# Optimization experiments

Measured on AMD Instinct MI355X. Metric: run time of the kernel, lower is better.

## Reference

```python
import jax, jax.numpy as jnp
import numpy as np

LN_EPS = 1e-3  # keras LayerNormalization default


def setup_inputs() -> dict:
    key = jax.random.key(0)
    k1, k2, k3 = jax.random.split(key, 3)
    B, T, D, H = 64, 512, 256, 512
    inputs = jax.random.normal(k1, (B, T, D), dtype=jnp.float32)
    h0 = jnp.zeros((B, H), dtype=jnp.float32)
    Wx = jax.random.normal(k2, (D, H), dtype=jnp.float32) / np.sqrt(D)
    Wh = jax.random.normal(k3, (H, H), dtype=jnp.float32) / np.sqrt(H)
    b = jnp.zeros((H,), dtype=jnp.float32)
    gamma = jnp.ones((H,), dtype=jnp.float32)
    beta = jnp.zeros((H,), dtype=jnp.float32)
    return {"inputs": inputs, "h0": h0, "Wx": Wx, "Wh": Wh, "b": b,
            "gamma": gamma, "beta": beta}


def _layer_norm(x, gamma, beta):
    mu = jnp.mean(x, axis=-1, keepdims=True)
    var = jnp.mean(jnp.square(x - mu), axis=-1, keepdims=True)
    return (x - mu) * jax.lax.rsqrt(var + LN_EPS) * gamma + beta


def reference(inputs, h0, Wx, Wh, b, gamma, beta):
    # Precompute input projection for all timesteps: [B, T, H]
    xproj = jnp.einsum('btd,dh->bth', inputs, Wx) + b

    def step(h, xp_t):
        z = xp_t + h @ Wh                      # SimpleRNNCell, activation=None
        h_new = jnp.tanh(_layer_norm(z, gamma, beta))
        return h_new, h_new

    _, outs = jax.lax.scan(step, h0, jnp.swapaxes(xproj, 0, 1))
    return jnp.swapaxes(outs, 0, 1)            # [B, T, H]
```

## Files before the change

### kernel.cpp

```cpp
#include <hip/hip_runtime.h>
#include <cstdint>
#include <cstddef>

#define T_STEPS 512
#define D_DIM 256
#define H_DIM 512
#define B_SZ 64

#define NCG 4
#define CGW (H_DIM / NCG)
#define NTH 512


#define BM 64
#define BN 128
#define BK 32

__global__ __launch_bounds__(256)
void xproj_gemm(const float* __restrict__ A, const float* __restrict__ Bm,
                const float* __restrict__ bias, float* __restrict__ C,
                int M, int N, int K) {
    __shared__ float As[BK][BM];
    __shared__ float Bs[BK][BN];

    const int tid = threadIdx.x;
    const int tx = tid & 15;
    const int ty = tid >> 4;
    const int row0 = blockIdx.y * BM;
    const int col0 = blockIdx.x * BN;

    float acc[4][8];
    #pragma unroll
    for (int i = 0; i < 4; ++i)
        #pragma unroll
        for (int j = 0; j < 8; ++j) acc[i][j] = 0.0f;

    for (int kt = 0; kt < K; kt += BK) {
        #pragma unroll
        for (int i = 0; i < 2; ++i) {
            int q  = tid + i * 256;
            int m  = q >> 3;
            int k4 = (q & 7) << 2;
            float4 v = *(const float4*)&A[(size_t)(row0 + m) * K + kt + k4];
            As[k4 + 0][m] = v.x; As[k4 + 1][m] = v.y;
            As[k4 + 2][m] = v.z; As[k4 + 3][m] = v.w;
        }
        #pragma unroll
        for (int i = 0; i < 4; ++i) {
            int q  = tid + i * 256;
            int kk = q >> 5;
            int n4 = (q & 31) << 2;
            *(float4*)&Bs[kk][n4] = *(const float4*)&Bm[(size_t)(kt + kk) * N + col0 + n4];
        }
        __syncthreads();
        #pragma unroll
        for (int k = 0; k < BK; ++k) {
            float4 a  = *(const float4*)&As[k][ty << 2];
            float4 b0 = *(const float4*)&Bs[k][tx << 2];
            float4 b1 = *(const float4*)&Bs[k][(tx << 2) + 64];
            float av[4] = {a.x, a.y, a.z, a.w};
            float bv[8] = {b0.x, b0.y, b0.z, b0.w, b1.x, b1.y, b1.z, b1.w};
            #pragma unroll
            for (int i = 0; i < 4; ++i)
                #pragma unroll
                for (int j = 0; j < 8; ++j)
                    acc[i][j] = fmaf(av[i], bv[j], acc[i][j]);
        }
        __syncthreads();
    }

    float bv0[4], bv1[4];
    #pragma unroll
    for (int j = 0; j < 4; ++j) {
        bv0[j] = bias[col0 + (tx << 2) + j];
        bv1[j] = bias[col0 + (tx << 2) + 64 + j];
    }
    #pragma unroll
    for (int i = 0; i < 4; ++i) {
        int r = row0 + (ty << 2) + i;
        float4 o0 = make_float4(acc[i][0] + bv0[0], acc[i][1] + bv0[1],
                                acc[i][2] + bv0[2], acc[i][3] + bv0[3]);
        float4 o1 = make_float4(acc[i][4] + bv1[0], acc[i][5] + bv1[1],
                                acc[i][6] + bv1[2], acc[i][7] + bv1[3]);
        *(float4*)&C[(size_t)r * N + col0 + (tx << 2)]      = o0;
        *(float4*)&C[(size_t)r * N + col0 + (tx << 2) + 64] = o1;
    }
}

__device__ __forceinline__ float tanh_fast(float x) {
    float ax = fabsf(x);
    float e  = __expf(2.0f * ax);
    float t  = 1.0f - 2.0f / (e + 1.0f);
    return copysignf(t, x);
}

__global__ __launch_bounds__(NTH)
void rnn_scan3(const float* __restrict__ Wh, const float* __restrict__ h0,
               const float* __restrict__ gamma, const float* __restrict__ beta,
               float* __restrict__ out,
               unsigned long long* __restrict__ zbuf) {
    const int r   = blockIdx.x & (B_SZ - 1);
    const int cg  = blockIdx.x >> 6;
    const int tid = threadIdx.x;
    const int c   = tid & (CGW - 1);
    const int kc  = tid >> 7;

    __shared__ float h_s[H_DIM];
    __shared__ float part_s[NCG][CGW];
    __shared__ float wred_s[16];

    float w[128];
    #pragma unroll
    for (int j = 0; j < 128; ++j)
        w[j] = Wh[(size_t)(kc * 128 + j) * H_DIM + cg * CGW + c];

    h_s[tid] = h0[r * H_DIM + tid];
    const float g_own = gamma[tid];
    const float b_own = beta[tid];
    float* outrow = out + (size_t)r * T_STEPS * H_DIM;
    unsigned long long* zrow0 = zbuf + (size_t)(r * 2) * H_DIM;
    __syncthreads();

    for (int t = 0; t < T_STEPS; ++t) {
        unsigned long long* zrow = zrow0 + (size_t)(t & 1) * H_DIM;
        const unsigned int tag = (unsigned int)(t + 1);

        float xp = 0.0f;
        if (tid < CGW) xp = outrow[t * H_DIM + cg * CGW + tid];

        float acc = 0.0f;
        const float4* h4 = (const float4*)&h_s[kc * 128];
        #pragma unroll
        for (int j4 = 0; j4 < 32; ++j4) {
            float4 hv = h4[j4];
            acc = fmaf(w[4 * j4 + 0], hv.x, acc);
            acc = fmaf(w[4 * j4 + 1], hv.y, acc);
            acc = fmaf(w[4 * j4 + 2], hv.z, acc);
            acc = fmaf(w[4 * j4 + 3], hv.w, acc);
        }
        part_s[kc][c] = acc;
        __syncthreads();

        if (tid < CGW) {
            float z = xp + part_s[0][tid] + part_s[1][tid]
                         + part_s[2][tid] + part_s[3][tid];
            unsigned long long pkt =
                ((unsigned long long)tag << 32) | (unsigned long long)__float_as_uint(z);
            __hip_atomic_store(&zrow[cg * CGW + tid], pkt,
                               __ATOMIC_RELAXED, __HIP_MEMORY_SCOPE_AGENT);
        }

        unsigned long long pkt;
        do {
            pkt = __hip_atomic_load(&zrow[tid], __ATOMIC_RELAXED,
                                    __HIP_MEMORY_SCOPE_AGENT);
        } while ((unsigned int)(pkt >> 32) != tag);
        float z = __uint_as_float((unsigned int)pkt);

        float s = z, q = z * z;
        #pragma unroll
        for (int o = 32; o > 0; o >>= 1) {
            s += __shfl_down(s, o, 64);
            q += __shfl_down(q, o, 64);
        }
        const int wid = tid >> 6;
        if ((tid & 63) == 0) { wred_s[wid] = s; wred_s[8 + wid] = q; }
        __syncthreads();
        float S = 0.0f, Q = 0.0f;
        #pragma unroll
        for (int i = 0; i < 8; ++i) { S += wred_s[i]; Q += wred_s[8 + i]; }
        float mean = S * (1.0f / H_DIM);
        float var  = Q * (1.0f / H_DIM) - mean * mean;
        float rstd = rsqrtf(var + 1e-3f);

        float hn = tanh_fast((z - mean) * rstd * g_own + b_own);
        if (kc == cg) outrow[t * H_DIM + tid] = hn;
        h_s[tid] = hn;
        __syncthreads();
    }
}

extern "C" void kernel_launch(void* const* d_in, const int* in_sizes, int n_in,
                              void* d_out, int out_size, void* d_ws, size_t ws_size,
                              hipStream_t stream) {
    const float* inputs = (const float*)d_in[0];
    const float* h0     = (const float*)d_in[1];
    const float* Wx     = (const float*)d_in[2];
    const float* Wh     = (const float*)d_in[3];
    const float* bias   = (const float*)d_in[4];
    const float* gamma  = (const float*)d_in[5];
    const float* beta   = (const float*)d_in[6];
    float* out = (float*)d_out;

    unsigned long long* zbuf = (unsigned long long*)d_ws;

    const int M = B_SZ * T_STEPS;
    dim3 g1(H_DIM / BN, M / BM);
    xproj_gemm<<<g1, 256, 0, stream>>>(inputs, Wx, bias, out, M, H_DIM, D_DIM);

    rnn_scan3<<<B_SZ * NCG, NTH, 0, stream>>>(Wh, h0, gamma, beta, out, zbuf);
}
```

Measured before the change: 1.246 ms.

## Add fast-path polling with sc0 loads for cross-block exchange, prefetch xproj

Each z packet is now written to two buffers: a workgroup-scope store to a fast buffer and an agent-scope store to a slow buffer. Readers poll the fast buffer with raw sc0 global loads up to a cap, then fall back to agent-scope atomics for good once the cap is hit. The change also prefetches the next timestep's xproj value with a nontemporal load and splits the dot product across four accumulators for more ILP. It aims to cut inter-block synchronization latency on the serial scan, at the cost of relying on memory-coherence behavior that is not guaranteed across CUs.

```diff
diff --git a/kernel.cpp b/kernel.cpp
--- a/kernel.cpp
+++ b/kernel.cpp
@@ -10,6 +10,7 @@
 #define NCG 4
 #define CGW (H_DIM / NCG)
 #define NTH 512
+#define POLL_CAP 1024
 
 
 #define BM 64
@@ -94,11 +95,13 @@
     return copysignf(t, x);
 }
 
-__global__ __launch_bounds__(NTH)
-void rnn_scan3(const float* __restrict__ Wh, const float* __restrict__ h0,
+__global__ __launch_bounds__(NTH, 1)
+void rnn_scan7(const float* __restrict__ Wh, const float* __restrict__ h0,
                const float* __restrict__ gamma, const float* __restrict__ beta,
                float* __restrict__ out,
-               unsigned long long* __restrict__ zbuf) {
+               unsigned long long* __restrict__ zfast,
+               unsigned long long* __restrict__ zslow,
+               int fast_ok) {
     const int r   = blockIdx.x & (B_SZ - 1);
     const int cg  = blockIdx.x >> 6;
     const int tid = threadIdx.x;
@@ -118,25 +121,35 @@
     const float g_own = gamma[tid];
     const float b_own = beta[tid];
     float* outrow = out + (size_t)r * T_STEPS * H_DIM;
-    unsigned long long* zrow0 = zbuf + (size_t)(r * 2) * H_DIM;
+    unsigned long long* zfrow0 = zfast + (size_t)(r * 2) * H_DIM;
+    unsigned long long* zsrow0 = zslow + (size_t)(r * 2) * H_DIM;
+
+    int fastmode = fast_ok;
+    float xp_next = 0.0f;
+    if (tid < CGW)
+        xp_next = __builtin_nontemporal_load(&outrow[cg * CGW + tid]);
     __syncthreads();
 
     for (int t = 0; t < T_STEPS; ++t) {
-        unsigned long long* zrow = zrow0 + (size_t)(t & 1) * H_DIM;
+        const size_t par = (size_t)(t & 1) * H_DIM;
+        unsigned long long* zfrow = zfrow0 + par;
+        unsigned long long* zsrow = zsrow0 + par;
         const unsigned int tag = (unsigned int)(t + 1);
-
-        float xp = 0.0f;
-        if (tid < CGW) xp = outrow[t * H_DIM + cg * CGW + tid];
+        const float xp = xp_next;
 
         float acc = 0.0f;
-        const float4* h4 = (const float4*)&h_s[kc * 128];
-        #pragma unroll
-        for (int j4 = 0; j4 < 32; ++j4) {
-            float4 hv = h4[j4];
-            acc = fmaf(w[4 * j4 + 0], hv.x, acc);
-            acc = fmaf(w[4 * j4 + 1], hv.y, acc);
-            acc = fmaf(w[4 * j4 + 2], hv.z, acc);
-            acc = fmaf(w[4 * j4 + 3], hv.w, acc);
+        {
+            const float4* h4 = (const float4*)&h_s[kc * 128];
+            float a0 = 0.0f, a1 = 0.0f, a2 = 0.0f, a3 = 0.0f;
+            #pragma unroll
+            for (int j4 = 0; j4 < 32; ++j4) {
+                float4 hv = h4[j4];
+                a0 = fmaf(w[4 * j4 + 0], hv.x, a0);
+                a1 = fmaf(w[4 * j4 + 1], hv.y, a1);
+                a2 = fmaf(w[4 * j4 + 2], hv.z, a2);
+                a3 = fmaf(w[4 * j4 + 3], hv.w, a3);
+            }
+            acc = (a0 + a1) + (a2 + a3);
         }
         part_s[kc][c] = acc;
         __syncthreads();
@@ -146,15 +159,36 @@
                          + part_s[2][tid] + part_s[3][tid];
             unsigned long long pkt =
                 ((unsigned long long)tag << 32) | (unsigned long long)__float_as_uint(z);
-            __hip_atomic_store(&zrow[cg * CGW + tid], pkt,
+            __hip_atomic_store(&zfrow[cg * CGW + tid], pkt,
+                               __ATOMIC_RELAXED, __HIP_MEMORY_SCOPE_WORKGROUP);
+            __hip_atomic_store(&zsrow[cg * CGW + tid], pkt,
                                __ATOMIC_RELAXED, __HIP_MEMORY_SCOPE_AGENT);
         }
 
-        unsigned long long pkt;
-        do {
-            pkt = __hip_atomic_load(&zrow[tid], __ATOMIC_RELAXED,
-                                    __HIP_MEMORY_SCOPE_AGENT);
-        } while ((unsigned int)(pkt >> 32) != tag);
+        if (tid < CGW && t + 1 < T_STEPS)
+            xp_next = __builtin_nontemporal_load(
+                &outrow[(size_t)(t + 1) * H_DIM + cg * CGW + tid]);
+
+        unsigned long long pkt = 0;
+        bool got = false;
+        if (fastmode) {
+            const unsigned long long* fa = &zfrow[tid];
+            #pragma unroll 1
+            for (int it = 0; it < POLL_CAP; ++it) {
+                unsigned long long v;
+                asm volatile("global_load_dwordx2 %0, %1, off sc0\n\t"
+                             "s_waitcnt vmcnt(0)"
+                             : "=v"(v) : "v"(fa) : "memory");
+                if ((unsigned)(v >> 32) == tag) { pkt = v; got = true; break; }
+            }
+            if (!got) fastmode = 0;
+        }
+        if (!got) {
+            do {
+                pkt = __hip_atomic_load(&zsrow[tid], __ATOMIC_RELAXED,
+                                        __HIP_MEMORY_SCOPE_AGENT);
+            } while ((unsigned int)(pkt >> 32) != tag);
+        }
         float z = __uint_as_float((unsigned int)pkt);
 
         float s = z, q = z * z;
@@ -192,11 +226,17 @@
     const float* beta   = (const float*)d_in[6];
     float* out = (float*)d_out;
 
-    unsigned long long* zbuf = (unsigned long long*)d_ws;
-
     const int M = B_SZ * T_STEPS;
     dim3 g1(H_DIM / BN, M / BM);
     xproj_gemm<<<g1, 256, 0, stream>>>(inputs, Wx, bias, out, M, H_DIM, D_DIM);
 
-    rnn_scan3<<<B_SZ * NCG, NTH, 0, stream>>>(Wh, h0, gamma, beta, out, zbuf);
-}
+    const size_t zwords = (size_t)B_SZ * 2 * H_DIM;
+    unsigned long long* zbase = (unsigned long long*)d_ws;
+    if (ws_size >= 2 * zwords * sizeof(unsigned long long)) {
+        rnn_scan7<<<B_SZ * NCG, NTH, 0, stream>>>(Wh, h0, gamma, beta, out,
+                                                  zbase, zbase + zwords, 1);
+    } else {
+        rnn_scan7<<<B_SZ * NCG, NTH, 0, stream>>>(Wh, h0, gamma, beta, out,
+                                                  zbase, zbase, 0);
+    }
+}
```

Result: slower. 1.713 ms (+37.6%).
